# Optimization experiments

Hardware: AMD Instinct MI355X
Metric: run time of the kernel (lower is better)

## Reference

```python
import jax, jax.numpy as jnp
import numpy as np

HEADS = 12
EPS_RMS = 1e-6
EPS_LN = 1e-5


def _rms_inorm(x, w):
    # torch.std over spatial dims (unbiased, ddof=1); no mean subtraction
    std = jnp.std(x, axis=(2, 3), keepdims=True, ddof=1)
    return x / (std + EPS_RMS) * w[None, :, None, None]


def _layernorm(x, w, b):
    m = jnp.mean(x, axis=-1, keepdims=True)
    v = jnp.var(x, axis=-1, keepdims=True)
    return (x - m) / jnp.sqrt(v + EPS_LN) * w + b


def setup_inputs() -> dict:
    key = jax.random.key(0)
    ks = jax.random.split(key, 16)
    B, C, H, W = 8, 768, 64, 64
    hd = C // HEADS
    s = 0.02
    return {
        "x": jax.random.normal(ks[0], (B, C, H, W), jnp.float32),
        "bcs": jnp.zeros((1, 2), jnp.int32),
        "norm1_w": jnp.ones((C,), jnp.float32),
        "norm2_w": jnp.ones((C,), jnp.float32),
        "mlpn_w": jnp.ones((C,), jnp.float32),
        "Win": jax.random.normal(ks[1], (3 * C, C), jnp.float32) * s,
        "bin_": jnp.zeros((3 * C,), jnp.float32),
        "Wout": jax.random.normal(ks[2], (C, C), jnp.float32) * s,
        "bout": jnp.zeros((C,), jnp.float32),
        "qn_w": jnp.ones((hd,), jnp.float32),
        "qn_b": jnp.zeros((hd,), jnp.float32),
        "kn_w": jnp.ones((hd,), jnp.float32),
        "kn_b": jnp.zeros((hd,), jnp.float32),
        "gamma_att": jnp.full((C,), 1e-6, jnp.float32),
        "gamma_mlp": jnp.full((C,), 1e-6, jnp.float32),
        "W1": jax.random.normal(ks[3], (C, 4 * C), jnp.float32) * s,
        "b1": jnp.zeros((4 * C,), jnp.float32),
        "W2": jax.random.normal(ks[4], (4 * C, C), jnp.float32) * s,
        "b2": jnp.zeros((C,), jnp.float32),
    }


def reference(x, bcs, norm1_w, norm2_w, mlpn_w, Win, bin_, Wout, bout,
              qn_w, qn_b, kn_w, kn_b, gamma_att, gamma_mlp, W1, b1, W2, b2):
    B, C, H, W = x.shape
    hd = C // HEADS
    scale = 1.0 / jnp.sqrt(jnp.asarray(hd, x.dtype))

    h = _rms_inorm(x, norm1_w)
    # 1x1 conv QKV: [B, 3C, H, W]
    qkv = jnp.einsum('bchw,oc->bohw', h, Win) + bin_[None, :, None, None]
    # b (he c3) h w -> b he h w c3, then split into q,k,v of head_dim each
    qkv = qkv.reshape(B, HEADS, 3 * hd, H, W).transpose(0, 1, 3, 4, 2)
    q, k, v = jnp.split(qkv, 3, axis=-1)  # each [B, he, H, W, hd]
    q = _layernorm(q, qn_w, qn_b)
    k = _layernorm(k, kn_w, kn_b)

    # row attention: attend along W for each row h
    sx = jnp.einsum('bnhqc,bnhkc->bnhqk', q, k) * scale
    xx = jnp.einsum('bnhqk,bnhkc->bnhqc', jax.nn.softmax(sx, axis=-1), v)
    # column attention: attend along H for each column w
    sy = jnp.einsum('bnqwc,bnkwc->bnwqk', q, k) * scale
    xy = jnp.einsum('bnwqk,bnkwc->bnqwc', jax.nn.softmax(sy, axis=-1), v)

    a = (xx + xy) * 0.5  # [B, he, H, W, hd]
    a = a.transpose(0, 1, 4, 2, 3).reshape(B, C, H, W)
    a = _rms_inorm(a, norm2_w)
    a = jnp.einsum('bchw,oc->bohw', a, Wout) + bout[None, :, None, None]
    x1 = a * gamma_att[None, :, None, None] + x

    t = x1.transpose(0, 2, 3, 1)  # [B, H, W, C]
    m = jax.nn.gelu(t @ W1 + b1, approximate=False) @ W2 + b2
    m = m.transpose(0, 3, 1, 2)
    m = _rms_inorm(m, mlpn_w)
    return x1 + gamma_mlp[None, :, None, None] * m
```

## Files before the change

### kernel.cpp

```cpp
#include <hip/hip_runtime.h>

typedef __attribute__((ext_vector_type(8))) short short8;
typedef __attribute__((ext_vector_type(4))) float f32x4;
typedef __attribute__((ext_vector_type(4))) unsigned short u16x4;
typedef __attribute__((ext_vector_type(8))) unsigned short u16x8;

#define BDIM 8
#define CDIM 768
#define C3 2304
#define C4 3072
#define HEADS 12
#define HD 64
#define HWD 4096
#define TOKS 32768

__device__ __forceinline__ float bf2f(unsigned short u) {
    union { unsigned int i; float f; } x; x.i = ((unsigned int)u) << 16; return x.f;
}
__device__ __forceinline__ unsigned short f2bf(float f) {
    union { float f; unsigned int i; } x; x.f = f;
    unsigned int r = x.i + 0x7FFFu + ((x.i >> 16) & 1u);
    return (unsigned short)(r >> 16);
}

__device__ __forceinline__ void gload_lds16(const unsigned short* g, unsigned short* l) {
    __builtin_amdgcn_global_load_lds(
        (const __attribute__((address_space(1))) void*)g,
        (__attribute__((address_space(3))) void*)l, 16, 0, 0);
}

__global__ __launch_bounds__(256) void convert_f32_bf16(
    const float* __restrict__ src, unsigned short* __restrict__ dst, int n)
{
    int i = (blockIdx.x * 256 + threadIdx.x) * 4;
    if (i + 3 >= n + 4) return;
    if (i + 3 < n) {
        float4 v = *(const float4*)&src[i];
        dst[i + 0] = f2bf(v.x); dst[i + 1] = f2bf(v.y);
        dst[i + 2] = f2bf(v.z); dst[i + 3] = f2bf(v.w);
    }
}

__global__ __launch_bounds__(256) void transpose_w(
    const float* __restrict__ src, unsigned short* __restrict__ dst, int R, int Cc)
{
    const int n0 = blockIdx.x * 64, k0 = blockIdx.y * 64;
    __shared__ float t[64][65];
    #pragma unroll
    for (int s = 0; s < 16; ++s) {
        int flat = threadIdx.x + 256 * s;
        int i = flat >> 6, j = flat & 63;
        t[i][j] = src[(long)(k0 + i) * Cc + n0 + j];
    }
    __syncthreads();
    #pragma unroll
    for (int s = 0; s < 16; ++s) {
        int flat = threadIdx.x + 256 * s;
        int jn = flat >> 6, ik = flat & 63;
        dst[(long)(n0 + jn) * R + k0 + ik] = f2bf(t[ik][jn]);
    }
}

__global__ __launch_bounds__(256) void stats_spatial_f32(
    const float* __restrict__ x, const float* __restrict__ wgt,
    float* __restrict__ sout, float eps)
{
    const int bc = blockIdx.x;
    const int c = bc % CDIM;
    const float4* p4 = (const float4*)(x + (long)bc * HWD);
    float s = 0.f, ss = 0.f;
    #pragma unroll
    for (int k = 0; k < 4; ++k) {
        float4 v = p4[threadIdx.x + 256 * k];
        s  += v.x + v.y + v.z + v.w;
        ss += v.x * v.x + v.y * v.y + v.z * v.z + v.w * v.w;
    }
    #pragma unroll
    for (int m = 1; m < 64; m <<= 1) { s += __shfl_xor(s, m); ss += __shfl_xor(ss, m); }
    __shared__ float rs[4], rss[4];
    int w = threadIdx.x >> 6, lane = threadIdx.x & 63;
    if (lane == 0) { rs[w] = s; rss[w] = ss; }
    __syncthreads();
    if (threadIdx.x == 0) {
        float S = rs[0] + rs[1] + rs[2] + rs[3];
        float Q = rss[0] + rss[1] + rss[2] + rss[3];
        float var = (Q - S * S * (1.f / 4096.f)) * (1.f / 4095.f);
        sout[bc] = wgt[c] / (sqrtf(var) + eps);
    }
}

__global__ __launch_bounds__(256) void stats_spatial_bf16(
    const unsigned short* __restrict__ t, const float* __restrict__ wgt,
    float* __restrict__ sout, float eps)
{
    const int b = blockIdx.x / 12, cg = blockIdx.x % 12;
    const int sub = threadIdx.x & 15, tr = threadIdx.x >> 4;
    const unsigned short* base = t + (long)b * HWD * CDIM + cg * 64 + sub * 4;
    float s[4] = {0.f, 0.f, 0.f, 0.f}, q[4] = {0.f, 0.f, 0.f, 0.f};
    for (int i = 0; i < 256; ++i) {
        const int token = tr + 16 * i;
        u16x4 v = *(const u16x4*)(base + (long)token * CDIM);
        #pragma unroll
        for (int j = 0; j < 4; ++j) { float f = bf2f(v[j]); s[j] += f; q[j] += f * f; }
    }
    __shared__ float ssum[16][64], ssq[16][64];
    #pragma unroll
    for (int j = 0; j < 4; ++j) { ssum[tr][sub * 4 + j] = s[j]; ssq[tr][sub * 4 + j] = q[j]; }
    __syncthreads();
    if (threadIdx.x < 64) {
        const int c = threadIdx.x;
        float S = 0.f, Q = 0.f;
        #pragma unroll
        for (int r = 0; r < 16; ++r) { S += ssum[r][c]; Q += ssq[r][c]; }
        const float var = (Q - S * S * (1.f / 4096.f)) * (1.f / 4095.f);
        const int cglob = cg * 64 + c;
        sout[b * CDIM + cglob] = wgt[cglob] / (sqrtf(var) + eps);
    }
}

__global__ __launch_bounds__(256) void make_h(
    const float* __restrict__ x, const float* __restrict__ s1,
    unsigned short* __restrict__ h)
{
    const int hw0 = blockIdx.x * 64, c0 = blockIdx.y * 64, b = blockIdx.z;
    __shared__ float t[64][65];
    #pragma unroll
    for (int s = 0; s < 16; ++s) {
        int flat = threadIdx.x + 256 * s;
        int ci = flat >> 6, hj = flat & 63;
        t[ci][hj] = x[(long)(b * CDIM + c0 + ci) * HWD + hw0 + hj];
    }
    __syncthreads();
    #pragma unroll
    for (int s = 0; s < 16; ++s) {
        int flat = threadIdx.x + 256 * s;
        int hi = flat >> 6, cj = flat & 63;
        float v = t[cj][hi] * s1[b * CDIM + c0 + cj];
        h[(long)(b * HWD + hw0 + hi) * CDIM + c0 + cj] = f2bf(v);
    }
}

template<int GELU>
__global__ __launch_bounds__(512, 2) void gemm256(
    const unsigned short* __restrict__ A, const unsigned short* __restrict__ BT,
    const float* __restrict__ bias, unsigned short* __restrict__ out,
    int M, int N, int K)
{
    extern __shared__ unsigned short smem[];
    const int tid = threadIdx.x;
    const int lane = tid & 63, w = tid >> 6;
    const int wm = w >> 2, wn = w & 3;
    const int lr = lane & 15, g = lane >> 4;

    const int nwg = gridDim.x;
    const int logical = (blockIdx.x & 7) * (nwg >> 3) + (blockIdx.x >> 3);
    const int gnx = N >> 8;
    const int n0 = (logical % gnx) << 8;
    const int m0 = (logical / gnx) << 8;

    const int ka = (((tid & 3) ^ ((tid >> 3) & 3)) << 3);
    const int rA0 = tid >> 2, rA1 = (512 + tid) >> 2;
    const unsigned short* aS0 = A + (long)(m0 + rA0) * K + ka;
    const unsigned short* aS1 = A + (long)(m0 + rA1) * K + ka;
    const unsigned short* bS0 = BT + (long)(n0 + rA0) * K + ka;
    const unsigned short* bS1 = BT + (long)(n0 + rA1) * K + ka;
    unsigned short* dA0 = smem + ((tid & ~63) + 0) * 8;
    unsigned short* dA1 = smem + ((tid & ~63) + 512) * 8;
    unsigned short* dB0 = dA0 + 32768;
    unsigned short* dB1 = dA1 + 32768;

#define STAGE(slot) do { \
        gload_lds16(aS0, dA0 + (slot) * 8192); \
        gload_lds16(aS1, dA1 + (slot) * 8192); \
        gload_lds16(bS0, dB0 + (slot) * 8192); \
        gload_lds16(bS1, dB1 + (slot) * 8192); \
        aS0 += 32; aS1 += 32; bS0 += 32; bS1 += 32; } while (0)

    const int nsub = K >> 5;
    const int koff = ((g ^ ((lr >> 1) & 3)) << 3);
    const int arow = wm * 128 + lr;
    const int brow = wn * 64 + lr;

    f32x4 acc[8][4] = {};

    STAGE(0); STAGE(1); STAGE(2);
    asm volatile("s_waitcnt vmcnt(8)" ::: "memory");
    __builtin_amdgcn_s_barrier();

    for (int j = 0; j < nsub; ++j) {
        const int slot = j & 3;
        const unsigned short* aT = smem + slot * 8192;
        const unsigned short* bT = smem + 32768 + slot * 8192;

        short8 af[8], bf[4];
        #pragma unroll
        for (int ni = 0; ni < 4; ++ni) bf[ni] = *(const short8*)&bT[(brow + ni * 16) * 32 + koff];
        #pragma unroll
        for (int mi = 0; mi < 8; ++mi) af[mi] = *(const short8*)&aT[(arow + mi * 16) * 32 + koff];
        if (j + 3 < nsub) STAGE((j + 3) & 3);
        __builtin_amdgcn_s_setprio(1);
        #pragma unroll
        for (int mi = 0; mi < 8; ++mi)
            #pragma unroll
            for (int ni = 0; ni < 4; ++ni)
                acc[mi][ni] = __builtin_amdgcn_mfma_f32_16x16x32_bf16(af[mi], bf[ni], acc[mi][ni], 0, 0, 0);
        __builtin_amdgcn_s_setprio(0);
        const int rem = nsub - 2 - j;
        if (rem >= 2)      { asm volatile("s_waitcnt vmcnt(8)" ::: "memory"); }
        else if (rem == 1) { asm volatile("s_waitcnt vmcnt(4)" ::: "memory"); }
        else if (rem == 0) { asm volatile("s_waitcnt vmcnt(0)" ::: "memory"); }
        __builtin_amdgcn_s_barrier();
        __builtin_amdgcn_sched_barrier(0);
    }
#undef STAGE

    #pragma unroll
    for (int mi = 0; mi < 8; ++mi) {
        #pragma unroll
        for (int ni = 0; ni < 4; ++ni) {
            const int gcol = n0 + wn * 64 + ni * 16 + lr;
            const float bv = bias[gcol];
            #pragma unroll
            for (int r = 0; r < 4; ++r) {
                const int grow = m0 + wm * 128 + mi * 16 + g * 4 + r;
                float v = acc[mi][ni][r] + bv;
                if (GELU) v = 0.5f * v * (1.f + erff(v * 0.70710678118f));
                out[(long)grow * N + gcol] = f2bf(v);
            }
        }
    }
}

__global__ __launch_bounds__(256) void qk_layernorm(
    unsigned short* __restrict__ qkv,
    const float* __restrict__ qw, const float* __restrict__ qb,
    const float* __restrict__ kw, const float* __restrict__ kb)
{
    const int pairIdx = blockIdx.x * 16 + (threadIdx.x >> 4);
    const int token = pairIdx / HEADS, he = pairIdx % HEADS;
    const int c4 = (threadIdx.x & 15) * 4;
    const long base = (long)token * C3 + he * 192;
    #pragma unroll
    for (int which = 0; which < 2; ++which) {
        const long off = base + which * 64 + c4;
        u16x4 v = *(u16x4*)&qkv[off];
        float f[4];
        #pragma unroll
        for (int j = 0; j < 4; ++j) f[j] = bf2f(v[j]);
        float s = f[0] + f[1] + f[2] + f[3];
        float q = f[0] * f[0] + f[1] * f[1] + f[2] * f[2] + f[3] * f[3];
        #pragma unroll
        for (int m = 1; m < 16; m <<= 1) { s += __shfl_xor(s, m); q += __shfl_xor(q, m); }
        const float mean = s * (1.f / 64.f);
        const float var = q * (1.f / 64.f) - mean * mean;
        const float rstd = rsqrtf(var + 1e-5f);
        const float* W = which ? kw : qw;
        const float* Bv = which ? kb : qb;
        u16x4 o;
        #pragma unroll
        for (int j = 0; j < 4; ++j)
            o[j] = f2bf((f[j] - mean) * rstd * W[c4 + j] + Bv[c4 + j]);
        *(u16x4*)&qkv[off] = o;
    }
}

template<int AXIS>
__global__ __launch_bounds__(128) void attn_axial(
    const unsigned short* __restrict__ qkv, unsigned short* __restrict__ a)
{
    __shared__ unsigned short lds[2][2][64 * 72];
    const int tid = threadIdx.x;
    const int lane = tid & 63, w = tid >> 6;
    const int lineG = blockIdx.x * 2 + w;
    const int b = lineG / 768;
    const int rem = lineG - b * 768;
    const int he = rem >> 6, line = rem & 63;
    const int ts = (AXIS == 0) ? 1 : 64;
    const long token0 = (long)b * HWD + (AXIS == 0 ? line * 64 : line);
    const long qbase = token0 * C3 + he * 192;
    unsigned short* VT = &lds[w][0][0];
    unsigned short* P  = &lds[w][1][0];
    const int lr = lane & 15, g = lane >> 4;

    {
        const int keyr = lane >> 3, d8 = (lane & 7) << 3;
        #pragma unroll
        for (int it = 0; it < 8; ++it) {
            const int key = it * 8 + keyr;
            u16x8 v = *(const u16x8*)&qkv[qbase + (long)key * ts * C3 + 128 + d8];
            #pragma unroll
            for (int j = 0; j < 8; ++j) VT[(d8 + j) * 72 + key] = v[j];
        }
    }

    short8 qf[4][2], kf[4][2];
    #pragma unroll
    for (int i = 0; i < 4; ++i)
        #pragma unroll
        for (int kk = 0; kk < 2; ++kk) {
            const long rb = qbase + (long)(i * 16 + lr) * ts * C3 + kk * 32 + g * 8;
            qf[i][kk] = *(const short8*)&qkv[rb];
            kf[i][kk] = *(const short8*)&qkv[rb + 64];
        }

    f32x4 acc[4][4] = {};
    #pragma unroll
    for (int mi = 0; mi < 4; ++mi)
        #pragma unroll
        for (int ni = 0; ni < 4; ++ni) {
            acc[mi][ni] = __builtin_amdgcn_mfma_f32_16x16x32_bf16(qf[mi][0], kf[ni][0], acc[mi][ni], 0, 0, 0);
            acc[mi][ni] = __builtin_amdgcn_mfma_f32_16x16x32_bf16(qf[mi][1], kf[ni][1], acc[mi][ni], 0, 0, 0);
        }

    #pragma unroll
    for (int mi = 0; mi < 4; ++mi)
        #pragma unroll
        for (int r = 0; r < 4; ++r) {
            float mx = -1e30f;
            #pragma unroll
            for (int ni = 0; ni < 4; ++ni) {
                float v = acc[mi][ni][r] * 0.125f; acc[mi][ni][r] = v; mx = fmaxf(mx, v);
            }
            #pragma unroll
            for (int m = 1; m < 16; m <<= 1) mx = fmaxf(mx, __shfl_xor(mx, m));
            float s = 0.f;
            #pragma unroll
            for (int ni = 0; ni < 4; ++ni) {
                float e = __expf(acc[mi][ni][r] - mx); acc[mi][ni][r] = e; s += e;
            }
            #pragma unroll
            for (int m = 1; m < 16; m <<= 1) s += __shfl_xor(s, m);
            const float inv = 1.f / s;
            const int row = mi * 16 + 4 * g + r;
            #pragma unroll
            for (int ni = 0; ni < 4; ++ni)
                P[row * 72 + ni * 16 + lr] = f2bf(acc[mi][ni][r] * inv);
        }
    __syncthreads();

    short8 pa[4][2], vb[4][2];
    #pragma unroll
    for (int i = 0; i < 4; ++i)
        #pragma unroll
        for (int kk = 0; kk < 2; ++kk) {
            pa[i][kk] = *(const short8*)&P[(i * 16 + lr) * 72 + kk * 32 + g * 8];
            vb[i][kk] = *(const short8*)&VT[(i * 16 + lr) * 72 + kk * 32 + g * 8];
        }
    f32x4 o2[4][4] = {};
    #pragma unroll
    for (int mi = 0; mi < 4; ++mi)
        #pragma unroll
        for (int ni = 0; ni < 4; ++ni) {
            o2[mi][ni] = __builtin_amdgcn_mfma_f32_16x16x32_bf16(pa[mi][0], vb[ni][0], o2[mi][ni], 0, 0, 0);
            o2[mi][ni] = __builtin_amdgcn_mfma_f32_16x16x32_bf16(pa[mi][1], vb[ni][1], o2[mi][ni], 0, 0, 0);
        }

    #pragma unroll
    for (int mi = 0; mi < 4; ++mi)
        #pragma unroll
        for (int r = 0; r < 4; ++r) {
            const int q = mi * 16 + 4 * g + r;
            const long tok = token0 + (long)q * ts;
            #pragma unroll
            for (int ni = 0; ni < 4; ++ni) {
                const int d = ni * 16 + lr;
                const long addr = tok * CDIM + he * 64 + d;
                const float v = o2[mi][ni][r] * 0.5f;
                if (AXIS == 0) a[addr] = f2bf(v);
                else           a[addr] = f2bf(bf2f(a[addr]) + v);
            }
        }
}

__global__ __launch_bounds__(256) void scale_inplace(
    unsigned short* __restrict__ a, const float* __restrict__ s2)
{
    const long i = ((long)blockIdx.x * 256 + threadIdx.x) * 4;
    const int c = (int)(i % CDIM);
    const int b = (int)(i / ((long)CDIM * HWD));
    u16x4 v = *(u16x4*)&a[i];
    u16x4 o;
    #pragma unroll
    for (int j = 0; j < 4; ++j) o[j] = f2bf(bf2f(v[j]) * s2[b * CDIM + c + j]);
    *(u16x4*)&a[i] = o;
}

__global__ __launch_bounds__(256) void x1_combine(
    const unsigned short* __restrict__ o, const float* __restrict__ x,
    const float* __restrict__ gamma, float* __restrict__ dout,
    unsigned short* __restrict__ x1b)
{
    const int hw0 = blockIdx.x * 64, c0 = blockIdx.y * 64, b = blockIdx.z;
    __shared__ float t[64][65];
    #pragma unroll
    for (int s = 0; s < 16; ++s) {
        int flat = threadIdx.x + 256 * s;
        int i = flat >> 6, j = flat & 63;
        t[i][j] = bf2f(o[(long)(b * HWD + hw0 + i) * CDIM + c0 + j]);
    }
    __syncthreads();
    #pragma unroll
    for (int s = 0; s < 16; ++s) {
        int flat = threadIdx.x + 256 * s;
        int j = flat >> 6, i = flat & 63;
        const long xi = (long)(b * CDIM + c0 + j) * HWD + hw0 + i;
        float v = x[xi] + gamma[c0 + j] * t[i][j];
        dout[xi] = v;
        t[i][j] = v;
    }
    __syncthreads();
    #pragma unroll
    for (int s = 0; s < 16; ++s) {
        int flat = threadIdx.x + 256 * s;
        int i = flat >> 6, j = flat & 63;
        x1b[(long)(b * HWD + hw0 + i) * CDIM + c0 + j] = f2bf(t[i][j]);
    }
}

__global__ __launch_bounds__(256) void final_combine(
    const unsigned short* __restrict__ m, const float* __restrict__ gm,
    const float* __restrict__ s3, float* __restrict__ dout)
{
    const int hw0 = blockIdx.x * 64, c0 = blockIdx.y * 64, b = blockIdx.z;
    __shared__ float t[64][65];
    #pragma unroll
    for (int s = 0; s < 16; ++s) {
        int flat = threadIdx.x + 256 * s;
        int i = flat >> 6, j = flat & 63;
        t[i][j] = bf2f(m[(long)(b * HWD + hw0 + i) * CDIM + c0 + j]);
    }
    __syncthreads();
    #pragma unroll
    for (int s = 0; s < 16; ++s) {
        int flat = threadIdx.x + 256 * s;
        int j = flat >> 6, i = flat & 63;
        const long xi = (long)(b * CDIM + c0 + j) * HWD + hw0 + i;
        dout[xi] = dout[xi] + gm[c0 + j] * s3[b * CDIM + c0 + j] * t[i][j];
    }
}

extern "C" void kernel_launch(void* const* d_in, const int* in_sizes, int n_in,
                              void* d_out, int out_size, void* d_ws, size_t ws_size,
                              hipStream_t stream) {
    const float* x      = (const float*)d_in[0];
    const float* n1w    = (const float*)d_in[2];
    const float* n2w    = (const float*)d_in[3];
    const float* mlw    = (const float*)d_in[4];
    const float* Win    = (const float*)d_in[5];
    const float* bin    = (const float*)d_in[6];
    const float* Wout   = (const float*)d_in[7];
    const float* bout   = (const float*)d_in[8];
    const float* qn_w   = (const float*)d_in[9];
    const float* qn_b   = (const float*)d_in[10];
    const float* kn_w   = (const float*)d_in[11];
    const float* kn_b   = (const float*)d_in[12];
    const float* gatt   = (const float*)d_in[13];
    const float* gmlp   = (const float*)d_in[14];
    const float* W1     = (const float*)d_in[15];
    const float* b1     = (const float*)d_in[16];
    const float* W2     = (const float*)d_in[17];
    const float* b2     = (const float*)d_in[18];
    float* dout = (float*)d_out;
    char* ws = (char*)d_ws;

    unsigned short* wQ  = (unsigned short*)(ws);
    unsigned short* wO  = (unsigned short*)(ws + (4L << 20));
    unsigned short* w1t = (unsigned short*)(ws + (6L << 20));
    unsigned short* w2t = (unsigned short*)(ws + (11L << 20));
    float* s1 = (float*)(ws + (16L << 20));
    float* s2 = s1 + 6144;
    float* s3 = s2 + 6144;
    unsigned short* bufH = (unsigned short*)(ws + (17L << 20));
    unsigned short* bufQ = (unsigned short*)(ws + (65L << 20));
    unsigned short* bufA = (unsigned short*)(ws + (209L << 20));

    hipFuncSetAttribute((const void*)&gemm256<0>, hipFuncAttributeMaxDynamicSharedMemorySize, 131072);
    hipFuncSetAttribute((const void*)&gemm256<1>, hipFuncAttributeMaxDynamicSharedMemorySize, 131072);

    convert_f32_bf16<<<1728, 256, 0, stream>>>(Win, wQ, C3 * CDIM);
    convert_f32_bf16<<<576, 256, 0, stream>>>(Wout, wO, CDIM * CDIM);
    transpose_w<<<dim3(C4 / 64, CDIM / 64), 256, 0, stream>>>(W1, w1t, CDIM, C4);
    transpose_w<<<dim3(CDIM / 64, C4 / 64), 256, 0, stream>>>(W2, w2t, C4, CDIM);

    stats_spatial_f32<<<BDIM * CDIM, 256, 0, stream>>>(x, n1w, s1, 1e-6f);
    make_h<<<dim3(64, 12, 8), 256, 0, stream>>>(x, s1, bufH);

    gemm256<0><<<(TOKS / 256) * (C3 / 256), 512, 131072, stream>>>(bufH, wQ, bin, bufQ, TOKS, C3, CDIM);
    qk_layernorm<<<TOKS * HEADS / 16, 256, 0, stream>>>(bufQ, qn_w, qn_b, kn_w, kn_b);

    attn_axial<0><<<BDIM * HEADS * 64 / 2, 128, 0, stream>>>(bufQ, bufA);
    attn_axial<1><<<BDIM * HEADS * 64 / 2, 128, 0, stream>>>(bufQ, bufA);

    stats_spatial_bf16<<<BDIM * 12, 256, 0, stream>>>(bufA, n2w, s2, 1e-6f);
    scale_inplace<<<TOKS * CDIM / 1024, 256, 0, stream>>>(bufA, s2);
    gemm256<0><<<(TOKS / 256) * (CDIM / 256), 512, 131072, stream>>>(bufA, wO, bout, bufH, TOKS, CDIM, CDIM);
    x1_combine<<<dim3(64, 12, 8), 256, 0, stream>>>(bufH, x, gatt, dout, bufA);

    for (int ch = 0; ch < 2; ++ch) {
        const unsigned short* x1c = bufA + (long)ch * 16384 * CDIM;
        unsigned short* mc = bufH + (long)ch * 16384 * CDIM;
        gemm256<1><<<(16384 / 256) * (C4 / 256), 512, 131072, stream>>>(x1c, w1t, b1, bufQ, 16384, C4, CDIM);
        gemm256<0><<<(16384 / 256) * (CDIM / 256), 512, 131072, stream>>>(bufQ, w2t, b2, mc, 16384, CDIM, C4);
    }

    stats_spatial_bf16<<<BDIM * 12, 256, 0, stream>>>(bufH, mlw, s3, 1e-6f);
    final_combine<<<dim3(64, 12, 8), 256, 0, stream>>>(bufH, gmlp, s3, dout);
}
```

Measured before the change: 979.1 us.

## Restructure GEMM main loop into double-buffered 64-wide K tiles with split staging

```diff
diff --git a/kernel.cpp b/kernel.cpp
--- a/kernel.cpp
+++ b/kernel.cpp
@@ -159,60 +159,78 @@
     const int m0 = (logical / gnx) << 8;
 
     const int ka = (((tid & 3) ^ ((tid >> 3) & 3)) << 3);
-    const int rA0 = tid >> 2, rA1 = (512 + tid) >> 2;
-    const unsigned short* aS0 = A + (long)(m0 + rA0) * K + ka;
-    const unsigned short* aS1 = A + (long)(m0 + rA1) * K + ka;
-    const unsigned short* bS0 = BT + (long)(n0 + rA0) * K + ka;
-    const unsigned short* bS1 = BT + (long)(n0 + rA1) * K + ka;
-    unsigned short* dA0 = smem + ((tid & ~63) + 0) * 8;
-    unsigned short* dA1 = smem + ((tid & ~63) + 512) * 8;
-    unsigned short* dB0 = dA0 + 32768;
-    unsigned short* dB1 = dA1 + 32768;
-
-#define STAGE(slot) do { \
-        gload_lds16(aS0, dA0 + (slot) * 8192); \
-        gload_lds16(aS1, dA1 + (slot) * 8192); \
-        gload_lds16(bS0, dB0 + (slot) * 8192); \
-        gload_lds16(bS1, dB1 + (slot) * 8192); \
-        aS0 += 32; aS1 += 32; bS0 += 32; bS1 += 32; } while (0)
-
-    const int nsub = K >> 5;
+    const unsigned short* aS0 = A + (long)(m0 + (tid >> 2)) * K + ka;
+    const unsigned short* aS1 = A + (long)(m0 + 128 + (tid >> 2)) * K + ka;
+    const unsigned short* bS0 = BT + (long)(n0 + (tid >> 2)) * K + ka;
+    const unsigned short* bS1 = BT + (long)(n0 + 128 + (tid >> 2)) * K + ka;
+    unsigned short* dstA0 = smem + (tid & ~63) * 8;
+    unsigned short* dstA1 = dstA0 + 4096;
+    unsigned short* dstB0 = smem + 32768 + (tid & ~63) * 8;
+    unsigned short* dstB1 = dstB0 + 4096;
+
+#define STAGE_KK(BUF, KK) do { \
+        gload_lds16(aS0 + (KK) * 32, dstA0 + (BUF) * 16384 + (KK) * 8192); \
+        gload_lds16(aS1 + (KK) * 32, dstA1 + (BUF) * 16384 + (KK) * 8192); \
+        gload_lds16(bS0 + (KK) * 32, dstB0 + (BUF) * 16384 + (KK) * 8192); \
+        gload_lds16(bS1 + (KK) * 32, dstB1 + (BUF) * 16384 + (KK) * 8192); } while (0)
+#define ADV() do { aS0 += 64; aS1 += 64; bS0 += 64; bS1 += 64; } while (0)
+
+    const int nt = K >> 6;
     const int koff = ((g ^ ((lr >> 1) & 3)) << 3);
-    const int arow = wm * 128 + lr;
-    const int brow = wn * 64 + lr;
+    const unsigned short* baseA = smem + (wm * 128 + lr) * 32 + koff;
+    const unsigned short* baseB = smem + 32768 + (wn * 64 + lr) * 32 + koff;
 
     f32x4 acc[8][4] = {};
 
-    STAGE(0); STAGE(1); STAGE(2);
-    asm volatile("s_waitcnt vmcnt(8)" ::: "memory");
-    __builtin_amdgcn_s_barrier();
-
-    for (int j = 0; j < nsub; ++j) {
-        const int slot = j & 3;
-        const unsigned short* aT = smem + slot * 8192;
-        const unsigned short* bT = smem + 32768 + slot * 8192;
-
-        short8 af[8], bf[4];
-        #pragma unroll
-        for (int ni = 0; ni < 4; ++ni) bf[ni] = *(const short8*)&bT[(brow + ni * 16) * 32 + koff];
-        #pragma unroll
-        for (int mi = 0; mi < 8; ++mi) af[mi] = *(const short8*)&aT[(arow + mi * 16) * 32 + koff];
-        if (j + 3 < nsub) STAGE((j + 3) & 3);
-        __builtin_amdgcn_s_setprio(1);
-        #pragma unroll
-        for (int mi = 0; mi < 8; ++mi)
-            #pragma unroll
-            for (int ni = 0; ni < 4; ++ni)
-                acc[mi][ni] = __builtin_amdgcn_mfma_f32_16x16x32_bf16(af[mi], bf[ni], acc[mi][ni], 0, 0, 0);
-        __builtin_amdgcn_s_setprio(0);
-        const int rem = nsub - 2 - j;
-        if (rem >= 2)      { asm volatile("s_waitcnt vmcnt(8)" ::: "memory"); }
-        else if (rem == 1) { asm volatile("s_waitcnt vmcnt(4)" ::: "memory"); }
-        else if (rem == 0) { asm volatile("s_waitcnt vmcnt(0)" ::: "memory"); }
-        __builtin_amdgcn_s_barrier();
-        __builtin_amdgcn_sched_barrier(0);
-    }
-#undef STAGE
+    STAGE_KK(0, 0); STAGE_KK(0, 1); ADV();
+    STAGE_KK(1, 0); STAGE_KK(1, 1); ADV();
+
+#define TILE(BUF, WAITN, STG) do { \
+        asm volatile("s_waitcnt vmcnt(" #WAITN ")" ::: "memory"); \
+        __builtin_amdgcn_s_barrier(); \
+        __builtin_amdgcn_sched_barrier(0); \
+        short8 a0[8], b0[4], a1[8], b1[4]; \
+        _Pragma("unroll") \
+        for (int ni = 0; ni < 4; ++ni) b0[ni] = *(const short8*)(baseB + (BUF) * 16384 + ni * 512); \
+        _Pragma("unroll") \
+        for (int mi = 0; mi < 8; ++mi) a0[mi] = *(const short8*)(baseA + (BUF) * 16384 + mi * 512); \
+        asm volatile("s_waitcnt lgkmcnt(0)" ::: "memory"); \
+        __builtin_amdgcn_s_barrier(); \
+        __builtin_amdgcn_sched_barrier(0); \
+        if (STG) STAGE_KK(BUF, 0); \
+        _Pragma("unroll") \
+        for (int ni = 0; ni < 4; ++ni) b1[ni] = *(const short8*)(baseB + (BUF) * 16384 + 8192 + ni * 512); \
+        _Pragma("unroll") \
+        for (int mi = 0; mi < 8; ++mi) a1[mi] = *(const short8*)(baseA + (BUF) * 16384 + 8192 + mi * 512); \
+        __builtin_amdgcn_s_setprio(1); \
+        _Pragma("unroll") \
+        for (int mi = 0; mi < 8; ++mi) \
+            _Pragma("unroll") \
+            for (int ni = 0; ni < 4; ++ni) \
+                acc[mi][ni] = __builtin_amdgcn_mfma_f32_16x16x32_bf16(a0[mi], b0[ni], acc[mi][ni], 0, 0, 0); \
+        __builtin_amdgcn_s_setprio(0); \
+        asm volatile("s_waitcnt lgkmcnt(0)" ::: "memory"); \
+        __builtin_amdgcn_s_barrier(); \
+        __builtin_amdgcn_sched_barrier(0); \
+        if (STG) { STAGE_KK(BUF, 1); ADV(); } \
+        __builtin_amdgcn_s_setprio(1); \
+        _Pragma("unroll") \
+        for (int mi = 0; mi < 8; ++mi) \
+            _Pragma("unroll") \
+            for (int ni = 0; ni < 4; ++ni) \
+                acc[mi][ni] = __builtin_amdgcn_mfma_f32_16x16x32_bf16(a1[mi], b1[ni], acc[mi][ni], 0, 0, 0); \
+        __builtin_amdgcn_s_setprio(0); \
+    } while (0)
+
+    for (int t = 0; t + 2 < nt; t += 2) {
+        TILE(0, 8, 1);
+        TILE(1, 8, 1);
+    }
+    TILE(0, 8, 0);
+    TILE(1, 0, 0);
+#undef TILE
+#undef STAGE_KK
+#undef ADV
 
     #pragma unroll
     for (int mi = 0; mi < 8; ++mi) {
```

After: 1.043 ms. 1.07x slower.
